# Kernel optimization log

Hardware: AMD Instinct MI355X
Metric: run time of the kernel (lower is better)

## Reference

```python
import jax, jax.numpy as jnp
import numpy as np

HEADS = 12
HEAD_SIZE = 64
HIDDEN = 768


def _rope_tables(seqlen, dim, dtype):
    inv_freq = 1.0 / (10000.0 ** (jnp.arange(0, dim, 2, dtype=jnp.float32) / dim))
    t = jnp.arange(seqlen, dtype=jnp.float32)
    freqs = t[:, None] * inv_freq[None, :]  # [L, dim/2]
    return jnp.sin(freqs).astype(dtype), jnp.cos(freqs).astype(dtype)


def _apply_rope(x, sin, cos):
    # x: [B, L, H, D]; sin/cos: [L, D/2] -> broadcast as [1, L, 1, D/2]
    sin = sin[None, :, None, :]
    cos = cos[None, :, None, :]
    x1 = x[..., 0::2]
    x2 = x[..., 1::2]
    out1 = x1 * cos - x2 * sin
    out2 = x1 * sin + x2 * cos
    # interleave back: stack on new last axis then flatten
    return jnp.stack([out1, out2], axis=-1).reshape(x.shape)


def setup_inputs() -> dict:
    key = jax.random.key(0)
    k1, k2, k3 = jax.random.split(key, 3)
    B, L = 8, 512
    inputs = jax.random.normal(k1, (B, L, HIDDEN), dtype=jnp.float32)
    attention_mask = jnp.ones((B, L), dtype=jnp.int32)
    out_dim = HEADS * 2 * HEAD_SIZE
    W = jax.random.normal(k2, (HIDDEN, out_dim), dtype=jnp.float32) * (1.0 / np.sqrt(HIDDEN))
    b = jax.random.normal(k3, (out_dim,), dtype=jnp.float32) * 0.02
    return {"inputs": inputs, "W": W, "b": b, "attention_mask": attention_mask}


def reference(inputs, W, b, attention_mask):
    B, L, _ = inputs.shape
    x = inputs @ W + b  # [B, L, H*2*D]
    x = x.reshape(B, L, HEADS, 2, HEAD_SIZE)
    qw = x[..., 0, :]  # [B, L, H, D]
    kw = x[..., 1, :]
    sin, cos = _rope_tables(L, HEAD_SIZE, x.dtype)
    qw = _apply_rope(qw, sin, cos)
    kw = _apply_rope(kw, sin, cos)
    logits = jnp.einsum('bmhd,bnhd->bhmn', qw, kw) / np.sqrt(HEAD_SIZE)
    neg_inf = jnp.finfo(logits.dtype).min
    am = attention_mask.astype(bool)
    valid = am[:, None, None, :] & am[:, None, :, None]
    logits = jnp.where(valid, logits, neg_inf)
    tri = jnp.tril(jnp.ones((L, L), dtype=bool), k=-1)
    logits = jnp.where(tri[None, None, :, :], neg_inf, logits)
    return logits
```

## Files before the change

kernel.cpp:

```cpp
#include <hip/hip_runtime.h>
#include <hip/hip_bf16.h>
#include <math.h>

constexpr int BATCH  = 8;
constexpr int SEQ    = 512;
constexpr int HEADS  = 12;
constexpr int HSIZE  = 64;
constexpr int HIDDEN = 768;
constexpr int OUTD   = 1536;
constexpr int M      = BATCH * SEQ;
constexpr int BH     = BATCH * HEADS;

#define NEG_INF (-3.3895313892515355e38f)

typedef short  s16x8 __attribute__((ext_vector_type(8)));
typedef float  f32x4 __attribute__((ext_vector_type(4)));

__device__ __forceinline__ short f2bf(float f) {
    __hip_bfloat16 h = __float2bfloat16(f);
    return *reinterpret_cast<short*>(&h);
}

__global__ __launch_bounds__(256) void prep_kernel(
    const float* __restrict__ X,  short* __restrict__ Xb,
    const float* __restrict__ W,  short* __restrict__ Wt,
    float* __restrict__ sc_sin,   float* __restrict__ sc_cos)
{
    __shared__ short Ls[32][36];
    const int b   = blockIdx.x;
    const int tid = threadIdx.x;

    if (b < 1536) {
        const int t = b * 256 + tid;
        const float4 a = ((const float4*)X)[t * 2];
        const float4 c = ((const float4*)X)[t * 2 + 1];
        s16x8 o;
        o[0] = f2bf(a.x); o[1] = f2bf(a.y); o[2] = f2bf(a.z); o[3] = f2bf(a.w);
        o[4] = f2bf(c.x); o[5] = f2bf(c.y); o[6] = f2bf(c.z); o[7] = f2bf(c.w);
        ((s16x8*)Xb)[t] = o;
    } else if (b < 2688) {
        const int bid = b - 1536;
        const int nx = bid % 48, ky = bid / 48;
        const int r  = tid >> 3;
        const int c4 = (tid & 7) * 4;
        const float4 v = *(const float4*)(W + (size_t)(ky * 32 + r) * OUTD + nx * 32 + c4);
        Ls[r][c4 + 0] = f2bf(v.x); Ls[r][c4 + 1] = f2bf(v.y);
        Ls[r][c4 + 2] = f2bf(v.z); Ls[r][c4 + 3] = f2bf(v.w);
        __syncthreads();
        short o0 = Ls[c4 + 0][r], o1 = Ls[c4 + 1][r];
        short o2 = Ls[c4 + 2][r], o3 = Ls[c4 + 3][r];
        short* dst = Wt + (size_t)(nx * 32 + r) * HIDDEN + ky * 32 + c4;
        dst[0] = o0; dst[1] = o1; dst[2] = o2; dst[3] = o3;
    } else {
        const int t   = (b - 2688) * 256 + tid;
        const int pos = t >> 5, pi = t & 31;
        const float invf = exp2f((float)(2 * pi) * (-13.287712379549449f / 64.0f));
        const float ang  = (float)pos * invf;
        sc_sin[t] = sinf(ang);
        sc_cos[t] = cosf(ang);
    }
}

__global__ __launch_bounds__(256) void proj_mfma_kernel(
    const short* __restrict__ Xb,
    const short* __restrict__ Wt,
    const float* __restrict__ bias,
    const float* __restrict__ sc_sin,
    const float* __restrict__ sc_cos,
    short* __restrict__ Qb,
    short* __restrict__ Kb)
{
    union Sh {
        struct { short As[128 * 64]; short Bs[64 * 64]; } st;
        float epi[128 * 68];
    };
    __shared__ Sh sh;

    const int tid = threadIdx.x;
    const int l   = tid & 63;
    const int w   = tid >> 6;
    const int mBase = blockIdx.y * 128;
    const int nBase = blockIdx.x * 64;
    const int wm = w * 32;

    const int r0  = tid >> 3;
    const int g   = tid & 7;
    const int gsw = (g ^ (r0 & 7)) * 8;

    s16x8 ar[4], br[2];
#pragma unroll
    for (int p = 0; p < 4; ++p)
        ar[p] = *(const s16x8*)(Xb + (size_t)(mBase + r0 + p * 32) * HIDDEN + g * 8);
#pragma unroll
    for (int p = 0; p < 2; ++p)
        br[p] = *(const s16x8*)(Wt + (size_t)(nBase + r0 + p * 32) * HIDDEN + g * 8);

    f32x4 acc[2][4] = {};

    for (int k0 = 0; k0 < HIDDEN; k0 += 64) {
        __syncthreads();
#pragma unroll
        for (int p = 0; p < 4; ++p)
            *(s16x8*)(sh.st.As + (r0 + p * 32) * 64 + gsw) = ar[p];
#pragma unroll
        for (int p = 0; p < 2; ++p)
            *(s16x8*)(sh.st.Bs + (r0 + p * 32) * 64 + gsw) = br[p];
        __syncthreads();
        if (k0 + 64 < HIDDEN) {
#pragma unroll
            for (int p = 0; p < 4; ++p)
                ar[p] = *(const s16x8*)(Xb + (size_t)(mBase + r0 + p * 32) * HIDDEN + (k0 + 64) + g * 8);
#pragma unroll
            for (int p = 0; p < 2; ++p)
                br[p] = *(const s16x8*)(Wt + (size_t)(nBase + r0 + p * 32) * HIDDEN + (k0 + 64) + g * 8);
        }
#pragma unroll
        for (int s = 0; s < 2; ++s) {
            const int c = ((s * 4 + (l >> 4)) ^ (l & 7)) * 8;
            s16x8 af[2], bf[4];
#pragma unroll
            for (int i = 0; i < 2; ++i)
                af[i] = *(const s16x8*)(sh.st.As + (wm + i * 16 + (l & 15)) * 64 + c);
#pragma unroll
            for (int j = 0; j < 4; ++j)
                bf[j] = *(const s16x8*)(sh.st.Bs + (j * 16 + (l & 15)) * 64 + c);
#pragma unroll
            for (int i = 0; i < 2; ++i)
#pragma unroll
                for (int j = 0; j < 4; ++j)
                    acc[i][j] = __builtin_amdgcn_mfma_f32_16x16x32_bf16(
                        af[i], bf[j], acc[i][j], 0, 0, 0);
        }
    }

    __syncthreads();

    const int colL = l & 15, quad = l >> 4;
#pragma unroll
    for (int j = 0; j < 4; ++j) {
        const int nl = j * 16 + colL;
#pragma unroll
        for (int i = 0; i < 2; ++i)
#pragma unroll
            for (int r = 0; r < 4; ++r)
                sh.epi[(wm + i * 16 + quad * 4 + r) * 68 + nl] = acc[i][j][r];
    }
    __syncthreads();

    const int bb   = mBase >> 9;
    const int pos0 = mBase & 511;
    const int h    = nBase >> 7;
    const int slot = (nBase >> 6) & 1;
    short* dst = (slot ? Kb : Qb) + ((size_t)(bb * HEADS + h) * SEQ + pos0) * HSIZE;

#pragma unroll
    for (int p = 0; p < 4; ++p) {
        const int c    = tid + p * 256;
        const int mrow = c >> 3;
        const int ch   = c & 7;
        const int dloc = ch * 8;
        const int pos  = pos0 + mrow;

        const float* src = &sh.epi[mrow * 68 + dloc];
        const float4 v0 = *(const float4*)(src);
        const float4 v1 = *(const float4*)(src + 4);
        const float* bp = bias + nBase + dloc;
        const float4 b0 = *(const float4*)(bp);
        const float4 b1 = *(const float4*)(bp + 4);
        const float4 sn = *(const float4*)(sc_sin + pos * 32 + (dloc >> 1));
        const float4 cs = *(const float4*)(sc_cos + pos * 32 + (dloc >> 1));

        const float e0 = v0.x + b0.x, o0 = v0.y + b0.y;
        const float e1 = v0.z + b0.z, o1 = v0.w + b0.w;
        const float e2 = v1.x + b1.x, o2 = v1.y + b1.y;
        const float e3 = v1.z + b1.z, o3 = v1.w + b1.w;
        s16x8 ov;
        ov[0] = f2bf(e0 * cs.x - o0 * sn.x); ov[1] = f2bf(e0 * sn.x + o0 * cs.x);
        ov[2] = f2bf(e1 * cs.y - o1 * sn.y); ov[3] = f2bf(e1 * sn.y + o1 * cs.y);
        ov[4] = f2bf(e2 * cs.z - o2 * sn.z); ov[5] = f2bf(e2 * sn.z + o2 * cs.z);
        ov[6] = f2bf(e3 * cs.w - o3 * sn.w); ov[7] = f2bf(e3 * sn.w + o3 * cs.w);
        *(s16x8*)(dst + (size_t)mrow * HSIZE + dloc) = ov;
    }
}

__global__ __launch_bounds__(256) void qk_mfma_kernel(
    const short* __restrict__ Qb,
    const short* __restrict__ Kb,
    const int*   __restrict__ am,
    float* __restrict__ out)
{
    const int bh = blockIdx.z;
    const int bb = bh / HEADS;
    const int m0 = blockIdx.y * 128;
    const int n0 = blockIdx.x * 128;
    const int tid = threadIdx.x;

    if (m0 >= n0 + 128) {
        const float4 ninf = make_float4(NEG_INF, NEG_INF, NEG_INF, NEG_INF);
        float* base = out + ((size_t)bh * SEQ + m0) * SEQ + n0;
        const int c = (tid & 31) * 4;
#pragma unroll
        for (int r = 0; r < 16; ++r) {
            const int row = r * 8 + (tid >> 5);
            *(float4*)(base + (size_t)row * SEQ + c) = ninf;
        }
        return;
    }

    __shared__ short Qs[128 * 64];
    __shared__ short Ks[128 * 64];
    __shared__ __align__(16) int amR[128];
    __shared__ __align__(16) int amC[128];

    const int l = tid & 63;
    const int w = tid >> 6;
    if (tid < 128)      amR[tid]       = am[bb * SEQ + m0 + tid];
    else                amC[tid - 128] = am[bb * SEQ + n0 + (tid - 128)];

    const int r0  = tid >> 3;
    const int g   = tid & 7;
    const int gsw = (g ^ (r0 & 7)) * 8;
#pragma unroll
    for (int p = 0; p < 4; ++p) {
        const int row = r0 + p * 32;
        const s16x8 qv = *(const s16x8*)(Qb + ((size_t)bh * SEQ + m0 + row) * HSIZE + g * 8);
        const s16x8 kv = *(const s16x8*)(Kb + ((size_t)bh * SEQ + n0 + row) * HSIZE + g * 8);
        *(s16x8*)(Qs + row * 64 + gsw) = qv;
        *(s16x8*)(Ks + row * 64 + gsw) = kv;
    }
    __syncthreads();

    const int wm = (w & 1) * 64;
    const int wn = (w >> 1) * 64;
    f32x4 acc[4][4] = {};
#pragma unroll
    for (int s = 0; s < 2; ++s) {
        const int c = ((s * 4 + (l >> 4)) ^ (l & 7)) * 8;
        s16x8 qf[4], kf[4];
#pragma unroll
        for (int i = 0; i < 4; ++i) {
            qf[i] = *(const s16x8*)(Qs + (wm + i * 16 + (l & 15)) * 64 + c);
            kf[i] = *(const s16x8*)(Ks + (wn + i * 16 + (l & 15)) * 64 + c);
        }
#pragma unroll
        for (int i = 0; i < 4; ++i)
#pragma unroll
            for (int j = 0; j < 4; ++j)
                acc[i][j] = __builtin_amdgcn_mfma_f32_16x16x32_bf16(
                    qf[i], kf[j], acc[i][j], 0, 0, 0);
    }

    const int colL = l & 15, quad = l >> 4;
    int rm[4][4];
#pragma unroll
    for (int i = 0; i < 4; ++i)
#pragma unroll
        for (int r = 0; r < 4; ++r)
            rm[i][r] = amR[wm + i * 16 + quad * 4 + r];

#pragma unroll
    for (int j = 0; j < 4; ++j) {
        const int nl = wn + j * 16 + colL;
        const int ng = n0 + nl;
        const int an = amC[nl];
#pragma unroll
        for (int i = 0; i < 4; ++i) {
#pragma unroll
            for (int r = 0; r < 4; ++r) {
                const int ml = wm + i * 16 + quad * 4 + r;
                const int mg = m0 + ml;
                float v = acc[i][j][r] * 0.125f;
                if (ng < mg || !an || !rm[i][r]) v = NEG_INF;
                out[((size_t)bh * SEQ + mg) * SEQ + ng] = v;
            }
        }
    }
}

extern "C" void kernel_launch(void* const* d_in, const int* in_sizes, int n_in,
                              void* d_out, int out_size, void* d_ws, size_t ws_size,
                              hipStream_t stream) {
    const float* X    = (const float*)d_in[0];
    const float* W    = (const float*)d_in[1];
    const float* bias = (const float*)d_in[2];
    const int*   am   = (const int*)d_in[3];
    float* out = (float*)d_out;

    char* ws = (char*)d_ws;
    short* Xb = (short*)(ws);
    short* Wt = (short*)(ws + 6291456);
    short* Qb = (short*)(ws + 8650752);
    short* Kb = (short*)(ws + 14942208);
    float* sc_sin = (float*)(ws + 21233664);
    float* sc_cos = (float*)(ws + 21299200);

    prep_kernel<<<dim3(2752), 256, 0, stream>>>(X, Xb, W, Wt, sc_sin, sc_cos);
    proj_mfma_kernel<<<dim3(OUTD / 64, M / 128), 256, 0, stream>>>(
        Xb, Wt, bias, sc_sin, sc_cos, Qb, Kb);
    qk_mfma_kernel<<<dim3(SEQ / 128, SEQ / 128, BH), 256, 0, stream>>>(Qb, Kb, am, out);
}
```

Measured before the change: 172.3 us.

## Switch both GEMMs to 32x32x16 MFMA with direct global operand loads

```diff
diff --git a/kernel.cpp b/kernel.cpp
--- a/kernel.cpp
+++ b/kernel.cpp
@@ -13,8 +13,8 @@
 
 #define NEG_INF (-3.3895313892515355e38f)
 
-typedef short  s16x8 __attribute__((ext_vector_type(8)));
-typedef float  f32x4 __attribute__((ext_vector_type(4)));
+typedef short  s16x8  __attribute__((ext_vector_type(8)));
+typedef float  f32x16 __attribute__((ext_vector_type(16)));
 
 __device__ __forceinline__ short f2bf(float f) {
     __hip_bfloat16 h = __float2bfloat16(f);
@@ -70,80 +70,38 @@
     short* __restrict__ Qb,
     short* __restrict__ Kb)
 {
-    union Sh {
-        struct { short As[128 * 64]; short Bs[64 * 64]; } st;
-        float epi[128 * 68];
-    };
-    __shared__ Sh sh;
+    __shared__ float epi[128 * 68];
 
     const int tid = threadIdx.x;
     const int l   = tid & 63;
     const int w   = tid >> 6;
     const int mBase = blockIdx.y * 128;
     const int nBase = blockIdx.x * 64;
-    const int wm = w * 32;
-
-    const int r0  = tid >> 3;
-    const int g   = tid & 7;
-    const int gsw = (g ^ (r0 & 7)) * 8;
-
-    s16x8 ar[4], br[2];
-#pragma unroll
-    for (int p = 0; p < 4; ++p)
-        ar[p] = *(const s16x8*)(Xb + (size_t)(mBase + r0 + p * 32) * HIDDEN + g * 8);
-#pragma unroll
-    for (int p = 0; p < 2; ++p)
-        br[p] = *(const s16x8*)(Wt + (size_t)(nBase + r0 + p * 32) * HIDDEN + g * 8);
-
-    f32x4 acc[2][4] = {};
-
-    for (int k0 = 0; k0 < HIDDEN; k0 += 64) {
-        __syncthreads();
-#pragma unroll
-        for (int p = 0; p < 4; ++p)
-            *(s16x8*)(sh.st.As + (r0 + p * 32) * 64 + gsw) = ar[p];
-#pragma unroll
-        for (int p = 0; p < 2; ++p)
-            *(s16x8*)(sh.st.Bs + (r0 + p * 32) * 64 + gsw) = br[p];
-        __syncthreads();
-        if (k0 + 64 < HIDDEN) {
-#pragma unroll
-            for (int p = 0; p < 4; ++p)
-                ar[p] = *(const s16x8*)(Xb + (size_t)(mBase + r0 + p * 32) * HIDDEN + (k0 + 64) + g * 8);
-#pragma unroll
-            for (int p = 0; p < 2; ++p)
-                br[p] = *(const s16x8*)(Wt + (size_t)(nBase + r0 + p * 32) * HIDDEN + (k0 + 64) + g * 8);
-        }
-#pragma unroll
-        for (int s = 0; s < 2; ++s) {
-            const int c = ((s * 4 + (l >> 4)) ^ (l & 7)) * 8;
-            s16x8 af[2], bf[4];
-#pragma unroll
-            for (int i = 0; i < 2; ++i)
-                af[i] = *(const s16x8*)(sh.st.As + (wm + i * 16 + (l & 15)) * 64 + c);
-#pragma unroll
-            for (int j = 0; j < 4; ++j)
-                bf[j] = *(const s16x8*)(sh.st.Bs + (j * 16 + (l & 15)) * 64 + c);
-#pragma unroll
-            for (int i = 0; i < 2; ++i)
-#pragma unroll
-                for (int j = 0; j < 4; ++j)
-                    acc[i][j] = __builtin_amdgcn_mfma_f32_16x16x32_bf16(
-                        af[i], bf[j], acc[i][j], 0, 0, 0);
-        }
-    }
-
-    __syncthreads();
-
-    const int colL = l & 15, quad = l >> 4;
-#pragma unroll
-    for (int j = 0; j < 4; ++j) {
-        const int nl = j * 16 + colL;
-#pragma unroll
-        for (int i = 0; i < 2; ++i)
-#pragma unroll
-            for (int r = 0; r < 4; ++r)
-                sh.epi[(wm + i * 16 + quad * 4 + r) * 68 + nl] = acc[i][j][r];
+    const int wm  = w * 32;
+    const int lm  = l & 31;
+    const int kh  = (l >> 5) * 8;
+
+    const short* aptr  = Xb + (size_t)(mBase + wm + lm) * HIDDEN + kh;
+    const short* bptr0 = Wt + (size_t)(nBase +      lm) * HIDDEN + kh;
+    const short* bptr1 = Wt + (size_t)(nBase + 32 + lm) * HIDDEN + kh;
+
+    f32x16 acc0 = {}, acc1 = {};
+
+#pragma unroll 4
+    for (int k0 = 0; k0 < HIDDEN; k0 += 16) {
+        const s16x8 a  = *(const s16x8*)(aptr  + k0);
+        const s16x8 b0 = *(const s16x8*)(bptr0 + k0);
+        const s16x8 b1 = *(const s16x8*)(bptr1 + k0);
+        acc0 = __builtin_amdgcn_mfma_f32_32x32x16_bf16(a, b0, acc0, 0, 0, 0);
+        acc1 = __builtin_amdgcn_mfma_f32_32x32x16_bf16(a, b1, acc1, 0, 0, 0);
+    }
+
+    const int rbase = wm + 4 * (l >> 5);
+#pragma unroll
+    for (int reg = 0; reg < 16; ++reg) {
+        const int row = rbase + (reg & 3) + 8 * (reg >> 2);
+        epi[row * 68 +      lm] = acc0[reg];
+        epi[row * 68 + 32 + lm] = acc1[reg];
     }
     __syncthreads();
 
@@ -161,7 +119,7 @@
         const int dloc = ch * 8;
         const int pos  = pos0 + mrow;
 
-        const float* src = &sh.epi[mrow * 68 + dloc];
+        const float* src = &epi[mrow * 68 + dloc];
         const float4 v0 = *(const float4*)(src);
         const float4 v1 = *(const float4*)(src + 4);
         const float* bp = bias + nBase + dloc;
@@ -207,70 +165,53 @@
         return;
     }
 
-    __shared__ short Qs[128 * 64];
-    __shared__ short Ks[128 * 64];
     __shared__ __align__(16) int amR[128];
     __shared__ __align__(16) int amC[128];
-
-    const int l = tid & 63;
-    const int w = tid >> 6;
     if (tid < 128)      amR[tid]       = am[bb * SEQ + m0 + tid];
     else                amC[tid - 128] = am[bb * SEQ + n0 + (tid - 128)];
 
-    const int r0  = tid >> 3;
-    const int g   = tid & 7;
-    const int gsw = (g ^ (r0 & 7)) * 8;
-#pragma unroll
-    for (int p = 0; p < 4; ++p) {
-        const int row = r0 + p * 32;
-        const s16x8 qv = *(const s16x8*)(Qb + ((size_t)bh * SEQ + m0 + row) * HSIZE + g * 8);
-        const s16x8 kv = *(const s16x8*)(Kb + ((size_t)bh * SEQ + n0 + row) * HSIZE + g * 8);
-        *(s16x8*)(Qs + row * 64 + gsw) = qv;
-        *(s16x8*)(Ks + row * 64 + gsw) = kv;
-    }
-    __syncthreads();
-
+    const int l  = tid & 63;
+    const int w  = tid >> 6;
     const int wm = (w & 1) * 64;
     const int wn = (w >> 1) * 64;
-    f32x4 acc[4][4] = {};
-#pragma unroll
-    for (int s = 0; s < 2; ++s) {
-        const int c = ((s * 4 + (l >> 4)) ^ (l & 7)) * 8;
-        s16x8 qf[4], kf[4];
-#pragma unroll
-        for (int i = 0; i < 4; ++i) {
-            qf[i] = *(const s16x8*)(Qs + (wm + i * 16 + (l & 15)) * 64 + c);
-            kf[i] = *(const s16x8*)(Ks + (wn + i * 16 + (l & 15)) * 64 + c);
-        }
-#pragma unroll
-        for (int i = 0; i < 4; ++i)
-#pragma unroll
-            for (int j = 0; j < 4; ++j)
-                acc[i][j] = __builtin_amdgcn_mfma_f32_16x16x32_bf16(
-                    qf[i], kf[j], acc[i][j], 0, 0, 0);
-    }
-
-    const int colL = l & 15, quad = l >> 4;
-    int rm[4][4];
-#pragma unroll
-    for (int i = 0; i < 4; ++i)
-#pragma unroll
-        for (int r = 0; r < 4; ++r)
-            rm[i][r] = amR[wm + i * 16 + quad * 4 + r];
-
-#pragma unroll
-    for (int j = 0; j < 4; ++j) {
-        const int nl = wn + j * 16 + colL;
+    const int lm = l & 31;
+    const int kh = (l >> 5) * 8;
+
+    const short* qp0 = Qb + ((size_t)bh * SEQ + m0 + wm +      lm) * HSIZE + kh;
+    const short* qp1 = qp0 + 32 * HSIZE;
+    const short* kp0 = Kb + ((size_t)bh * SEQ + n0 + wn +      lm) * HSIZE + kh;
+    const short* kp1 = kp0 + 32 * HSIZE;
+
+    f32x16 acc00 = {}, acc01 = {}, acc10 = {}, acc11 = {};
+#pragma unroll
+    for (int k0 = 0; k0 < HSIZE; k0 += 16) {
+        const s16x8 q0 = *(const s16x8*)(qp0 + k0);
+        const s16x8 q1 = *(const s16x8*)(qp1 + k0);
+        const s16x8 kv0 = *(const s16x8*)(kp0 + k0);
+        const s16x8 kv1 = *(const s16x8*)(kp1 + k0);
+        acc00 = __builtin_amdgcn_mfma_f32_32x32x16_bf16(q0, kv0, acc00, 0, 0, 0);
+        acc01 = __builtin_amdgcn_mfma_f32_32x32x16_bf16(q0, kv1, acc01, 0, 0, 0);
+        acc10 = __builtin_amdgcn_mfma_f32_32x32x16_bf16(q1, kv0, acc10, 0, 0, 0);
+        acc11 = __builtin_amdgcn_mfma_f32_32x32x16_bf16(q1, kv1, acc11, 0, 0, 0);
+    }
+    __syncthreads();
+
+    const int rb = 4 * (l >> 5);
+    const f32x16* accs[2][2] = { { &acc00, &acc01 }, { &acc10, &acc11 } };
+#pragma unroll
+    for (int j = 0; j < 2; ++j) {
+        const int nl = wn + j * 32 + lm;
         const int ng = n0 + nl;
         const int an = amC[nl];
 #pragma unroll
-        for (int i = 0; i < 4; ++i) {
-#pragma unroll
-            for (int r = 0; r < 4; ++r) {
-                const int ml = wm + i * 16 + quad * 4 + r;
+        for (int i = 0; i < 2; ++i) {
+            const f32x16 a = *accs[i][j];
+#pragma unroll
+            for (int reg = 0; reg < 16; ++reg) {
+                const int ml = wm + i * 32 + rb + (reg & 3) + 8 * (reg >> 2);
                 const int mg = m0 + ml;
-                float v = acc[i][j][r] * 0.125f;
-                if (ng < mg || !an || !rm[i][r]) v = NEG_INF;
+                float v = a[reg] * 0.125f;
+                if (ng < mg || !an || !amR[ml]) v = NEG_INF;
                 out[((size_t)bh * SEQ + mg) * SEQ + ng] = v;
             }
         }
```

Result: slower. 193.7 us (+12.4%).
